# Optimization experiments

Measured on AMD Instinct MI355X. Metric: run time of the kernel, lower is better.

## Reference

```python
import jax, jax.numpy as jnp
import numpy as np

B, N, C = 16, 196608, 2

def setup_inputs() -> dict:
    key = jax.random.key(0)
    k1, k2, k3, k4, k5 = jax.random.split(key, 5)
    return {
        "r": jax.random.normal(k1, (B, N, C), dtype=jnp.float32),
        "w": jax.random.uniform(k2, (B, N, 2), dtype=jnp.float32),
        "J_p": jax.random.normal(k3, (B, N, C, 6), dtype=jnp.float32),
        "J_d": jax.random.uniform(k4, (B, N, C, 1), dtype=jnp.float32),
        "lmbda": jax.random.uniform(k5, (B, 1, 1), dtype=jnp.float32),
    }

def reference(r, w, J_p, J_d, lmbda):
    # r: (B,N,C)  w: (B,N,2)  J_p: (B,N,C,6)  J_d: (B,N,C,1)  lmbda: (B,1,1)
    conf = w[..., 0:1]                                  # (B,N,1)
    node_lambda = w[..., 1:2]                           # (B,N,1)
    conf4 = conf[..., None]                             # (B,N,1,1)
    Jd = J_d[..., 0]                                    # (B,N,C)

    # Gauss-Newton blocks (sum-over-N reductions of tiny outer products)
    H_pp = jnp.einsum('bnki,bnkj->bij', J_p, conf4 * J_p)        # (B,6,6)
    H_pd = jnp.einsum('bnki,bnkj->bnij', J_p, conf4 * J_d)       # (B,N,6,1)
    H_dd = jnp.einsum('bnk,bnk->bn', Jd, conf * Jd)[..., None]   # (B,N,1)
    wr = conf * r                                                # (B,N,C)
    g_p = jnp.einsum('bnki,bnk->bi', J_p, wr)[..., None]         # (B,6,1)
    g_d = jnp.einsum('bnk,bnk->bn', Jd, wr)[..., None]           # (B,N,1)

    eye6 = jnp.eye(6, dtype=H_pp.dtype)[None]                    # (1,6,6)
    H_pp = H_pp + lmbda * eye6                                   # LM damping on pose block

    # Depth block damping + safe inverse
    H_dd_safe = jnp.maximum(H_dd + lmbda + node_lambda, 1e-4)    # (B,N,1)
    inv_H_dd = 1.0 / H_dd_safe                                   # (B,N,1)

    # Schur complement: H_eff = H_pp - sum_n H_pd invHdd H_pd^T
    H_pd_invHdd = H_pd * inv_H_dd[..., None]                     # (B,N,6,1)
    term = jnp.einsum('bnik,bnjk->bij', H_pd_invHdd, H_pd)       # (B,6,6)
    H_eff = H_pp - term + (0.01 + 0.001) * eye6                  # eye*0.01 then ridge 0.001
    g_eff = g_p - jnp.sum(H_pd_invHdd * g_d[..., None], axis=1)  # (B,6,1)

    delta_pose = jnp.linalg.solve(H_eff, g_eff)                  # (B,6,1)
    dp = delta_pose[..., 0]                                      # (B,6)

    # Back-substitute depths
    v = jnp.einsum('bnij,bi->bnj', H_pd, dp)                     # (B,N,1)
    delta_depth = inv_H_dd * (g_d - v)                           # (B,N,1)

    delta_pose_out = jnp.clip(dp, -2.0, 2.0)                     # (B,6)
    return (delta_pose_out, delta_depth)
```

## Files before the change

### kernel.cpp

```cpp
#include <hip/hip_runtime.h>


constexpr int NACC = 27;

__device__ __forceinline__ void accum_point(
    const float ja[6], const float jb[6],
    float r0, float r1, float conf, float nlam, float jd0, float jd1,
    float lam, float* __restrict__ A, float* __restrict__ g)
{
    float h[6], gp[6];
#pragma unroll
    for (int i = 0; i < 6; ++i) {
        h[i]  = conf * (ja[i] * jd0 + jb[i] * jd1);
        gp[i] = conf * (ja[i] * r0 + jb[i] * r1);
    }
    const float hdd = conf * (jd0 * jd0 + jd1 * jd1);
    const float inv = 1.0f / fmaxf(hdd + lam + nlam, 1e-4f);
    const float gd  = conf * (jd0 * r0 + jd1 * r1);
    const float gdinv = gd * inv;
    int idx = 0;
#pragma unroll
    for (int i = 0; i < 6; ++i) {
        const float hii = h[i] * inv;
#pragma unroll
        for (int j = i; j < 6; ++j) {
            A[idx] += conf * (ja[i] * ja[j] + jb[i] * jb[j]) - hii * h[j];
            ++idx;
        }
        g[i] += gp[i] - h[i] * gdinv;
    }
}

constexpr int LDS_PITCH = 65;
constexpr int LDS_WAVE  = 6 * LDS_PITCH;

__device__ __forceinline__ void lds_fence()
{
    asm volatile("s_waitcnt lgkmcnt(0)" ::: "memory");
    __builtin_amdgcn_sched_barrier(0);
}

__global__ __launch_bounds__(256) void dba_reduce(
    const float* __restrict__ r, const float* __restrict__ w,
    const float* __restrict__ J_p, const float* __restrict__ J_d,
    const float* __restrict__ lmbda, float* __restrict__ acc, int N)
{
    __shared__ float4 sJ[4][LDS_WAVE];
    const int b = blockIdx.y;
    const float lam = lmbda[b];
    const int lane = threadIdx.x & 63;
    const int wave = threadIdx.x >> 6;
    float4* __restrict__ ldsW = sJ[wave];

    float A[21];
    float g[6];
#pragma unroll
    for (int i = 0; i < 21; ++i) A[i] = 0.f;
#pragma unroll
    for (int i = 0; i < 6; ++i) g[i] = 0.f;

    const size_t basePt = (size_t)b * (size_t)N;
    const int P  = N >> 1;
    const int PF = P & ~63;

    const float4* __restrict__ r4  = (const float4*)r   + (basePt >> 1);
    const float4* __restrict__ w4  = (const float4*)w   + (basePt >> 1);
    const float4* __restrict__ jd4 = (const float4*)J_d + (basePt >> 1);
    const float4* __restrict__ jp4 = (const float4*)J_p + basePt * 3;

    const int gw = blockIdx.x * 4 + wave;
    const int chunkStride = gridDim.x * 4;

    for (int pr0 = gw << 6; pr0 < PF; pr0 += chunkStride << 6) {
        const float4 rv = r4[pr0 + lane];
        const float4 wv = w4[pr0 + lane];
        const float4 jd = jd4[pr0 + lane];

        const float4* __restrict__ jpseg = jp4 + (size_t)pr0 * 6;
#pragma unroll
        for (int k = 0; k < 6; ++k) {
            const int gg = (k << 6) + lane;
            const float4 q = jpseg[gg];
            const int p = gg / 6;
            const int s = gg - p * 6;
            ldsW[s * LDS_PITCH + p] = q;
        }
        lds_fence();

        {
            const float4 J0 = ldsW[0 * LDS_PITCH + lane];
            const float4 J1 = ldsW[1 * LDS_PITCH + lane];
            const float4 J2 = ldsW[2 * LDS_PITCH + lane];
            const float ja[6] = {J0.x, J0.y, J0.z, J0.w, J1.x, J1.y};
            const float jb[6] = {J1.z, J1.w, J2.x, J2.y, J2.z, J2.w};
            accum_point(ja, jb, rv.x, rv.y, wv.x, wv.y, jd.x, jd.y, lam, A, g);
        }
        {
            const float4 J3 = ldsW[3 * LDS_PITCH + lane];
            const float4 J4 = ldsW[4 * LDS_PITCH + lane];
            const float4 J5 = ldsW[5 * LDS_PITCH + lane];
            const float ja[6] = {J3.x, J3.y, J3.z, J3.w, J4.x, J4.y};
            const float jb[6] = {J4.z, J4.w, J5.x, J5.y, J5.z, J5.w};
            accum_point(ja, jb, rv.z, rv.w, wv.z, wv.w, jd.z, jd.w, lam, A, g);
        }
    }

    for (int pr = PF + (int)(blockIdx.x * blockDim.x + threadIdx.x); pr < P;
         pr += (int)(gridDim.x * blockDim.x)) {
        const size_t pt = basePt + ((size_t)pr << 1);
        const float4 rv = *(const float4*)(r + pt * 2);
        const float4 wv = *(const float4*)(w + pt * 2);
        const float4 jd = *(const float4*)(J_d + pt * 2);
        const float4* jp = (const float4*)(J_p + pt * 12);
        const float4 q0 = jp[0], q1 = jp[1], q2 = jp[2];
        const float4 q3 = jp[3], q4 = jp[4], q5 = jp[5];
        {
            const float ja[6] = {q0.x, q0.y, q0.z, q0.w, q1.x, q1.y};
            const float jb[6] = {q1.z, q1.w, q2.x, q2.y, q2.z, q2.w};
            accum_point(ja, jb, rv.x, rv.y, wv.x, wv.y, jd.x, jd.y, lam, A, g);
        }
        {
            const float ja[6] = {q3.x, q3.y, q3.z, q3.w, q4.x, q4.y};
            const float jb[6] = {q4.z, q4.w, q5.x, q5.y, q5.z, q5.w};
            accum_point(ja, jb, rv.z, rv.w, wv.z, wv.w, jd.z, jd.w, lam, A, g);
        }
    }

    float v[NACC];
#pragma unroll
    for (int i = 0; i < 21; ++i) v[i] = A[i];
#pragma unroll
    for (int i = 0; i < 6; ++i) v[21 + i] = g[i];

#pragma unroll
    for (int off = 32; off > 0; off >>= 1) {
#pragma unroll
        for (int i = 0; i < NACC; ++i) v[i] += __shfl_down(v[i], off, 64);
    }

    __shared__ float sred[4][NACC];
    if (lane == 0) {
#pragma unroll
        for (int i = 0; i < NACC; ++i) sred[wave][i] = v[i];
    }
    __syncthreads();
    if (threadIdx.x < NACC) {
        const float s = sred[0][threadIdx.x] + sred[1][threadIdx.x] +
                        sred[2][threadIdx.x] + sred[3][threadIdx.x];
        atomicAdd(&acc[b * 32 + threadIdx.x], s);
    }
}

__global__ void dba_solve(const float* __restrict__ acc,
                          const float* __restrict__ lmbda,
                          float* __restrict__ pose_out,
                          float* __restrict__ dp_ws, int B)
{
    const int b = blockIdx.x * blockDim.x + threadIdx.x;
    if (b >= B) return;
    float M[6][7];
    const float* a = acc + b * 32;
    int idx = 0;
#pragma unroll
    for (int i = 0; i < 6; ++i) {
#pragma unroll
        for (int j = i; j < 6; ++j) {
            const float t = a[idx++];
            M[i][j] = t;
            M[j][i] = t;
        }
    }
#pragma unroll
    for (int i = 0; i < 6; ++i) M[i][6] = a[21 + i];
    const float lam = lmbda[b];
#pragma unroll
    for (int i = 0; i < 6; ++i) M[i][i] += lam + 0.011f;

#pragma unroll
    for (int k = 0; k < 6; ++k) {
        const float piv = 1.0f / M[k][k];
#pragma unroll
        for (int j = 0; j < 7; ++j) M[k][j] *= piv;
#pragma unroll
        for (int i = 0; i < 6; ++i) {
            if (i == k) continue;
            const float f = M[i][k];
#pragma unroll
            for (int j = 0; j < 7; ++j) M[i][j] -= f * M[k][j];
        }
    }
#pragma unroll
    for (int i = 0; i < 6; ++i) {
        const float x = M[i][6];
        dp_ws[b * 6 + i] = x;
        pose_out[b * 6 + i] = fminf(fmaxf(x, -2.0f), 2.0f);
    }
}

__device__ __forceinline__ float depth_point(
    const float ja[6], const float jb[6], const float* __restrict__ dp,
    float r0, float r1, float conf, float nlam, float jd0, float jd1, float lam)
{
    float v = 0.f;
#pragma unroll
    for (int i = 0; i < 6; ++i)
        v += (ja[i] * jd0 + jb[i] * jd1) * dp[i];
    v *= conf;
    const float hdd = conf * (jd0 * jd0 + jd1 * jd1);
    const float inv = 1.0f / fmaxf(hdd + lam + nlam, 1e-4f);
    const float gd  = conf * (jd0 * r0 + jd1 * r1);
    return inv * (gd - v);
}

__global__ __launch_bounds__(256) void dba_depth(
    const float* __restrict__ r, const float* __restrict__ w,
    const float* __restrict__ J_p, const float* __restrict__ J_d,
    const float* __restrict__ lmbda, const float* __restrict__ dp_ws,
    float* __restrict__ depth_out, int N)
{
    __shared__ float4 sJ[4][LDS_WAVE];
    const int b = blockIdx.y;
    const float lam = lmbda[b];
    const int lane = threadIdx.x & 63;
    const int wave = threadIdx.x >> 6;
    float4* __restrict__ ldsW = sJ[wave];

    float dp[6];
#pragma unroll
    for (int i = 0; i < 6; ++i) dp[i] = dp_ws[b * 6 + i];

    const size_t basePt = (size_t)b * (size_t)N;
    const int P  = N >> 1;
    const int PF = P & ~63;

    const float4* __restrict__ r4  = (const float4*)r   + (basePt >> 1);
    const float4* __restrict__ w4  = (const float4*)w   + (basePt >> 1);
    const float4* __restrict__ jd4 = (const float4*)J_d + (basePt >> 1);
    const float4* __restrict__ jp4 = (const float4*)J_p + basePt * 3;
    float2* __restrict__ out2 = (float2*)depth_out + (basePt >> 1);

    const int gw = blockIdx.x * 4 + wave;
    const int chunkStride = gridDim.x * 4;

    for (int pr0 = gw << 6; pr0 < PF; pr0 += chunkStride << 6) {
        const float4 rv = r4[pr0 + lane];
        const float4 wv = w4[pr0 + lane];
        const float4 jd = jd4[pr0 + lane];

        const float4* __restrict__ jpseg = jp4 + (size_t)pr0 * 6;
#pragma unroll
        for (int k = 0; k < 6; ++k) {
            const int gg = (k << 6) + lane;
            const float4 q = jpseg[gg];
            const int p = gg / 6;
            const int s = gg - p * 6;
            ldsW[s * LDS_PITCH + p] = q;
        }
        lds_fence();

        float2 outv;
        {
            const float4 J0 = ldsW[0 * LDS_PITCH + lane];
            const float4 J1 = ldsW[1 * LDS_PITCH + lane];
            const float4 J2 = ldsW[2 * LDS_PITCH + lane];
            const float ja[6] = {J0.x, J0.y, J0.z, J0.w, J1.x, J1.y};
            const float jb[6] = {J1.z, J1.w, J2.x, J2.y, J2.z, J2.w};
            outv.x = depth_point(ja, jb, dp, rv.x, rv.y, wv.x, wv.y, jd.x, jd.y, lam);
        }
        {
            const float4 J3 = ldsW[3 * LDS_PITCH + lane];
            const float4 J4 = ldsW[4 * LDS_PITCH + lane];
            const float4 J5 = ldsW[5 * LDS_PITCH + lane];
            const float ja[6] = {J3.x, J3.y, J3.z, J3.w, J4.x, J4.y};
            const float jb[6] = {J4.z, J4.w, J5.x, J5.y, J5.z, J5.w};
            outv.y = depth_point(ja, jb, dp, rv.z, rv.w, wv.z, wv.w, jd.z, jd.w, lam);
        }
        out2[pr0 + lane] = outv;
    }

    for (int pr = PF + (int)(blockIdx.x * blockDim.x + threadIdx.x); pr < P;
         pr += (int)(gridDim.x * blockDim.x)) {
        const size_t pt = basePt + ((size_t)pr << 1);
        const float4 rv = *(const float4*)(r + pt * 2);
        const float4 wv = *(const float4*)(w + pt * 2);
        const float4 jd = *(const float4*)(J_d + pt * 2);
        const float4* jp = (const float4*)(J_p + pt * 12);
        const float4 q0 = jp[0], q1 = jp[1], q2 = jp[2];
        const float4 q3 = jp[3], q4 = jp[4], q5 = jp[5];
        float2 outv;
        {
            const float ja[6] = {q0.x, q0.y, q0.z, q0.w, q1.x, q1.y};
            const float jb[6] = {q1.z, q1.w, q2.x, q2.y, q2.z, q2.w};
            outv.x = depth_point(ja, jb, dp, rv.x, rv.y, wv.x, wv.y, jd.x, jd.y, lam);
        }
        {
            const float ja[6] = {q3.x, q3.y, q3.z, q3.w, q4.x, q4.y};
            const float jb[6] = {q4.z, q4.w, q5.x, q5.y, q5.z, q5.w};
            outv.y = depth_point(ja, jb, dp, rv.z, rv.w, wv.z, wv.w, jd.z, jd.w, lam);
        }
        *(float2*)(depth_out + pt) = outv;
    }
}

extern "C" void kernel_launch(void* const* d_in, const int* in_sizes, int n_in,
                              void* d_out, int out_size, void* d_ws, size_t ws_size,
                              hipStream_t stream)
{
    const float* r   = (const float*)d_in[0];
    const float* w   = (const float*)d_in[1];
    const float* J_p = (const float*)d_in[2];
    const float* J_d = (const float*)d_in[3];
    const float* lmb = (const float*)d_in[4];
    const int B = in_sizes[4];
    const int N = in_sizes[0] / (B * 2);

    float* acc   = (float*)d_ws;
    float* dp_ws = (float*)d_ws + B * 32;
    float* out   = (float*)d_out;

    hipMemsetAsync(acc, 0, B * 32 * sizeof(float), stream);

    dim3 grid(96, B);
    dba_reduce<<<grid, 256, 0, stream>>>(r, w, J_p, J_d, lmb, acc, N);
    dba_solve<<<1, 64, 0, stream>>>(acc, lmb, out, dp_ws, B);
    dba_depth<<<grid, 256, 0, stream>>>(r, w, J_p, J_d, lmb, dp_ws, out + B * 6, N);
}
```

Measured before the change: 309.6 us.

## Software-pipeline global loads with register prefetch and nontemporal hints

Both the reduction and depth kernels now issue the global loads for the next chunk (r, w, J_d and six J_p vectors) into registers before processing the current chunk, overlapping memory latency with the LDS transpose and arithmetic. LDS write and read addresses are precomputed once outside the loop. All streaming loads, and the depth store, use nontemporal builtins. This raises register pressure and may lower occupancy. The nontemporal hints may also stop the second kernel from reusing data left in cache by the first.

```diff
diff --git a/kernel.cpp b/kernel.cpp
--- a/kernel.cpp
+++ b/kernel.cpp
@@ -1,5 +1,12 @@
 #include <hip/hip_runtime.h>
 
+
+using f4 = __attribute__((ext_vector_type(4))) float;
+using f2 = __attribute__((ext_vector_type(2))) float;
+
+__device__ __forceinline__ f4 ntload4(const f4* p) {
+    return __builtin_nontemporal_load(p);
+}
 
 constexpr int NACC = 27;
 
@@ -45,12 +52,12 @@
     const float* __restrict__ J_p, const float* __restrict__ J_d,
     const float* __restrict__ lmbda, float* __restrict__ acc, int N)
 {
-    __shared__ float4 sJ[4][LDS_WAVE];
+    __shared__ f4 sJ[4][LDS_WAVE];
     const int b = blockIdx.y;
     const float lam = lmbda[b];
     const int lane = threadIdx.x & 63;
     const int wave = threadIdx.x >> 6;
-    float4* __restrict__ ldsW = sJ[wave];
+    f4* __restrict__ ldsW = sJ[wave];
 
     float A[21];
     float g[6];
@@ -63,45 +70,85 @@
     const int P  = N >> 1;
     const int PF = P & ~63;
 
-    const float4* __restrict__ r4  = (const float4*)r   + (basePt >> 1);
-    const float4* __restrict__ w4  = (const float4*)w   + (basePt >> 1);
-    const float4* __restrict__ jd4 = (const float4*)J_d + (basePt >> 1);
-    const float4* __restrict__ jp4 = (const float4*)J_p + basePt * 3;
+    const f4* __restrict__ r4  = (const f4*)r   + (basePt >> 1);
+    const f4* __restrict__ w4  = (const f4*)w   + (basePt >> 1);
+    const f4* __restrict__ jd4 = (const f4*)J_d + (basePt >> 1);
+    const f4* __restrict__ jp4 = (const f4*)J_p + basePt * 3;
 
     const int gw = blockIdx.x * 4 + wave;
-    const int chunkStride = gridDim.x * 4;
-
-    for (int pr0 = gw << 6; pr0 < PF; pr0 += chunkStride << 6) {
-        const float4 rv = r4[pr0 + lane];
-        const float4 wv = w4[pr0 + lane];
-        const float4 jd = jd4[pr0 + lane];
-
-        const float4* __restrict__ jpseg = jp4 + (size_t)pr0 * 6;
-#pragma unroll
-        for (int k = 0; k < 6; ++k) {
-            const int gg = (k << 6) + lane;
-            const float4 q = jpseg[gg];
-            const int p = gg / 6;
-            const int s = gg - p * 6;
-            ldsW[s * LDS_PITCH + p] = q;
-        }
-        lds_fence();
-
-        {
-            const float4 J0 = ldsW[0 * LDS_PITCH + lane];
-            const float4 J1 = ldsW[1 * LDS_PITCH + lane];
-            const float4 J2 = ldsW[2 * LDS_PITCH + lane];
-            const float ja[6] = {J0.x, J0.y, J0.z, J0.w, J1.x, J1.y};
-            const float jb[6] = {J1.z, J1.w, J2.x, J2.y, J2.z, J2.w};
-            accum_point(ja, jb, rv.x, rv.y, wv.x, wv.y, jd.x, jd.y, lam, A, g);
-        }
-        {
-            const float4 J3 = ldsW[3 * LDS_PITCH + lane];
-            const float4 J4 = ldsW[4 * LDS_PITCH + lane];
-            const float4 J5 = ldsW[5 * LDS_PITCH + lane];
-            const float ja[6] = {J3.x, J3.y, J3.z, J3.w, J4.x, J4.y};
-            const float jb[6] = {J4.z, J4.w, J5.x, J5.y, J5.z, J5.w};
-            accum_point(ja, jb, rv.z, rv.w, wv.z, wv.w, jd.z, jd.w, lam, A, g);
+    const int step = (gridDim.x * 4) << 6;
+
+    f4* wadr[6];
+#pragma unroll
+    for (int k = 0; k < 6; ++k) {
+        const int gg = (k << 6) + lane;
+        const int p = gg / 6;
+        const int s = gg - p * 6;
+        wadr[k] = &ldsW[s * LDS_PITCH + p];
+    }
+    const f4* radr0 = &ldsW[0 * LDS_PITCH + lane];
+    const f4* radr1 = &ldsW[1 * LDS_PITCH + lane];
+    const f4* radr2 = &ldsW[2 * LDS_PITCH + lane];
+    const f4* radr3 = &ldsW[3 * LDS_PITCH + lane];
+    const f4* radr4 = &ldsW[4 * LDS_PITCH + lane];
+    const f4* radr5 = &ldsW[5 * LDS_PITCH + lane];
+
+    int pr0 = gw << 6;
+    if (pr0 < PF) {
+        const f4* jps = jp4 + (size_t)pr0 * 6;
+        f4 c_rv = ntload4(r4 + pr0 + lane);
+        f4 c_wv = ntload4(w4 + pr0 + lane);
+        f4 c_jd = ntload4(jd4 + pr0 + lane);
+        f4 c_q0 = ntload4(jps + 0 * 64 + lane);
+        f4 c_q1 = ntload4(jps + 1 * 64 + lane);
+        f4 c_q2 = ntload4(jps + 2 * 64 + lane);
+        f4 c_q3 = ntload4(jps + 3 * 64 + lane);
+        f4 c_q4 = ntload4(jps + 4 * 64 + lane);
+        f4 c_q5 = ntload4(jps + 5 * 64 + lane);
+
+        for (; pr0 < PF; pr0 += step) {
+            const int nxt = (pr0 + step < PF) ? (pr0 + step) : pr0;
+            const f4* jpn = jp4 + (size_t)nxt * 6;
+            f4 n_rv = ntload4(r4 + nxt + lane);
+            f4 n_wv = ntload4(w4 + nxt + lane);
+            f4 n_jd = ntload4(jd4 + nxt + lane);
+            f4 n_q0 = ntload4(jpn + 0 * 64 + lane);
+            f4 n_q1 = ntload4(jpn + 1 * 64 + lane);
+            f4 n_q2 = ntload4(jpn + 2 * 64 + lane);
+            f4 n_q3 = ntload4(jpn + 3 * 64 + lane);
+            f4 n_q4 = ntload4(jpn + 4 * 64 + lane);
+            f4 n_q5 = ntload4(jpn + 5 * 64 + lane);
+
+            *wadr[0] = c_q0;
+            *wadr[1] = c_q1;
+            *wadr[2] = c_q2;
+            *wadr[3] = c_q3;
+            *wadr[4] = c_q4;
+            *wadr[5] = c_q5;
+            lds_fence();
+
+            {
+                const f4 J0 = *radr0;
+                const f4 J1 = *radr1;
+                const f4 J2 = *radr2;
+                const float ja[6] = {J0[0], J0[1], J0[2], J0[3], J1[0], J1[1]};
+                const float jb[6] = {J1[2], J1[3], J2[0], J2[1], J2[2], J2[3]};
+                accum_point(ja, jb, c_rv[0], c_rv[1], c_wv[0], c_wv[1],
+                            c_jd[0], c_jd[1], lam, A, g);
+            }
+            {
+                const f4 J3 = *radr3;
+                const f4 J4 = *radr4;
+                const f4 J5 = *radr5;
+                const float ja[6] = {J3[0], J3[1], J3[2], J3[3], J4[0], J4[1]};
+                const float jb[6] = {J4[2], J4[3], J5[0], J5[1], J5[2], J5[3]};
+                accum_point(ja, jb, c_rv[2], c_rv[3], c_wv[2], c_wv[3],
+                            c_jd[2], c_jd[3], lam, A, g);
+            }
+
+            c_rv = n_rv; c_wv = n_wv; c_jd = n_jd;
+            c_q0 = n_q0; c_q1 = n_q1; c_q2 = n_q2;
+            c_q3 = n_q3; c_q4 = n_q4; c_q5 = n_q5;
         }
     }
 
@@ -218,12 +265,12 @@
     const float* __restrict__ lmbda, const float* __restrict__ dp_ws,
     float* __restrict__ depth_out, int N)
 {
-    __shared__ float4 sJ[4][LDS_WAVE];
+    __shared__ f4 sJ[4][LDS_WAVE];
     const int b = blockIdx.y;
     const float lam = lmbda[b];
     const int lane = threadIdx.x & 63;
     const int wave = threadIdx.x >> 6;
-    float4* __restrict__ ldsW = sJ[wave];
+    f4* __restrict__ ldsW = sJ[wave];
 
     float dp[6];
 #pragma unroll
@@ -233,49 +280,89 @@
     const int P  = N >> 1;
     const int PF = P & ~63;
 
-    const float4* __restrict__ r4  = (const float4*)r   + (basePt >> 1);
-    const float4* __restrict__ w4  = (const float4*)w   + (basePt >> 1);
-    const float4* __restrict__ jd4 = (const float4*)J_d + (basePt >> 1);
-    const float4* __restrict__ jp4 = (const float4*)J_p + basePt * 3;
-    float2* __restrict__ out2 = (float2*)depth_out + (basePt >> 1);
+    const f4* __restrict__ r4  = (const f4*)r   + (basePt >> 1);
+    const f4* __restrict__ w4  = (const f4*)w   + (basePt >> 1);
+    const f4* __restrict__ jd4 = (const f4*)J_d + (basePt >> 1);
+    const f4* __restrict__ jp4 = (const f4*)J_p + basePt * 3;
+    f2* __restrict__ out2 = (f2*)depth_out + (basePt >> 1);
 
     const int gw = blockIdx.x * 4 + wave;
-    const int chunkStride = gridDim.x * 4;
-
-    for (int pr0 = gw << 6; pr0 < PF; pr0 += chunkStride << 6) {
-        const float4 rv = r4[pr0 + lane];
-        const float4 wv = w4[pr0 + lane];
-        const float4 jd = jd4[pr0 + lane];
-
-        const float4* __restrict__ jpseg = jp4 + (size_t)pr0 * 6;
-#pragma unroll
-        for (int k = 0; k < 6; ++k) {
-            const int gg = (k << 6) + lane;
-            const float4 q = jpseg[gg];
-            const int p = gg / 6;
-            const int s = gg - p * 6;
-            ldsW[s * LDS_PITCH + p] = q;
-        }
-        lds_fence();
-
-        float2 outv;
-        {
-            const float4 J0 = ldsW[0 * LDS_PITCH + lane];
-            const float4 J1 = ldsW[1 * LDS_PITCH + lane];
-            const float4 J2 = ldsW[2 * LDS_PITCH + lane];
-            const float ja[6] = {J0.x, J0.y, J0.z, J0.w, J1.x, J1.y};
-            const float jb[6] = {J1.z, J1.w, J2.x, J2.y, J2.z, J2.w};
-            outv.x = depth_point(ja, jb, dp, rv.x, rv.y, wv.x, wv.y, jd.x, jd.y, lam);
-        }
-        {
-            const float4 J3 = ldsW[3 * LDS_PITCH + lane];
-            const float4 J4 = ldsW[4 * LDS_PITCH + lane];
-            const float4 J5 = ldsW[5 * LDS_PITCH + lane];
-            const float ja[6] = {J3.x, J3.y, J3.z, J3.w, J4.x, J4.y};
-            const float jb[6] = {J4.z, J4.w, J5.x, J5.y, J5.z, J5.w};
-            outv.y = depth_point(ja, jb, dp, rv.z, rv.w, wv.z, wv.w, jd.z, jd.w, lam);
-        }
-        out2[pr0 + lane] = outv;
+    const int step = (gridDim.x * 4) << 6;
+
+    f4* wadr[6];
+#pragma unroll
+    for (int k = 0; k < 6; ++k) {
+        const int gg = (k << 6) + lane;
+        const int p = gg / 6;
+        const int s = gg - p * 6;
+        wadr[k] = &ldsW[s * LDS_PITCH + p];
+    }
+    const f4* radr0 = &ldsW[0 * LDS_PITCH + lane];
+    const f4* radr1 = &ldsW[1 * LDS_PITCH + lane];
+    const f4* radr2 = &ldsW[2 * LDS_PITCH + lane];
+    const f4* radr3 = &ldsW[3 * LDS_PITCH + lane];
+    const f4* radr4 = &ldsW[4 * LDS_PITCH + lane];
+    const f4* radr5 = &ldsW[5 * LDS_PITCH + lane];
+
+    int pr0 = gw << 6;
+    if (pr0 < PF) {
+        const f4* jps = jp4 + (size_t)pr0 * 6;
+        f4 c_rv = ntload4(r4 + pr0 + lane);
+        f4 c_wv = ntload4(w4 + pr0 + lane);
+        f4 c_jd = ntload4(jd4 + pr0 + lane);
+        f4 c_q0 = ntload4(jps + 0 * 64 + lane);
+        f4 c_q1 = ntload4(jps + 1 * 64 + lane);
+        f4 c_q2 = ntload4(jps + 2 * 64 + lane);
+        f4 c_q3 = ntload4(jps + 3 * 64 + lane);
+        f4 c_q4 = ntload4(jps + 4 * 64 + lane);
+        f4 c_q5 = ntload4(jps + 5 * 64 + lane);
+
+        for (; pr0 < PF; pr0 += step) {
+            const int nxt = (pr0 + step < PF) ? (pr0 + step) : pr0;
+            const f4* jpn = jp4 + (size_t)nxt * 6;
+            f4 n_rv = ntload4(r4 + nxt + lane);
+            f4 n_wv = ntload4(w4 + nxt + lane);
+            f4 n_jd = ntload4(jd4 + nxt + lane);
+            f4 n_q0 = ntload4(jpn + 0 * 64 + lane);
+            f4 n_q1 = ntload4(jpn + 1 * 64 + lane);
+            f4 n_q2 = ntload4(jpn + 2 * 64 + lane);
+            f4 n_q3 = ntload4(jpn + 3 * 64 + lane);
+            f4 n_q4 = ntload4(jpn + 4 * 64 + lane);
+            f4 n_q5 = ntload4(jpn + 5 * 64 + lane);
+
+            *wadr[0] = c_q0;
+            *wadr[1] = c_q1;
+            *wadr[2] = c_q2;
+            *wadr[3] = c_q3;
+            *wadr[4] = c_q4;
+            *wadr[5] = c_q5;
+            lds_fence();
+
+            f2 outv;
+            {
+                const f4 J0 = *radr0;
+                const f4 J1 = *radr1;
+                const f4 J2 = *radr2;
+                const float ja[6] = {J0[0], J0[1], J0[2], J0[3], J1[0], J1[1]};
+                const float jb[6] = {J1[2], J1[3], J2[0], J2[1], J2[2], J2[3]};
+                outv[0] = depth_point(ja, jb, dp, c_rv[0], c_rv[1], c_wv[0],
+                                      c_wv[1], c_jd[0], c_jd[1], lam);
+            }
+            {
+                const f4 J3 = *radr3;
+                const f4 J4 = *radr4;
+                const f4 J5 = *radr5;
+                const float ja[6] = {J3[0], J3[1], J3[2], J3[3], J4[0], J4[1]};
+                const float jb[6] = {J4[2], J4[3], J5[0], J5[1], J5[2], J5[3]};
+                outv[1] = depth_point(ja, jb, dp, c_rv[2], c_rv[3], c_wv[2],
+                                      c_wv[3], c_jd[2], c_jd[3], lam);
+            }
+            __builtin_nontemporal_store(outv, out2 + pr0 + lane);
+
+            c_rv = n_rv; c_wv = n_wv; c_jd = n_jd;
+            c_q0 = n_q0; c_q1 = n_q1; c_q2 = n_q2;
+            c_q3 = n_q3; c_q4 = n_q4; c_q5 = n_q5;
+        }
     }
 
     for (int pr = PF + (int)(blockIdx.x * blockDim.x + threadIdx.x); pr < P;
```

After: 305.0 us. About the same (-1.5%).
